# Kernel optimization log

Hardware: AMD Instinct MI355X
Metric: run time of the kernel (lower is better)

Reference implementation:

```python
import jax, jax.numpy as jnp
import numpy as np

WH, WW = 8, 8          # window_size
NUM_HEADS = 16
DIM = 512
NW = 64                # windows per image (mask leading dim)
BATCH = 16             # images
N = WH * WW            # tokens per window


def _relative_position_index():
    coords = np.stack(np.meshgrid(np.arange(WH), np.arange(WW), indexing='ij'))  # (2,Wh,Ww)
    cf = coords.reshape(2, -1)                                                   # (2,N)
    rel = cf[:, :, None] - cf[:, None, :]                                        # (2,N,N)
    rel = rel.transpose(1, 2, 0).astype(np.int64)                                # (N,N,2)
    rel[:, :, 0] += WH - 1
    rel[:, :, 1] += WW - 1
    rel[:, :, 0] *= 2 * WW - 1
    return jnp.asarray(rel.sum(-1), dtype=jnp.int32)                             # (N,N)


def setup_inputs() -> dict:
    key = jax.random.key(0)
    ks = jax.random.split(key, 8)
    B_ = BATCH * NW
    x = jax.random.normal(ks[0], (B_, N, DIM), dtype=jnp.float32)
    # 0 / -100 additive shift-style mask (Swin uses -100.0 for masked pairs)
    mraw = jax.random.uniform(ks[1], (NW, N, N))
    mask = jnp.where(mraw < 0.15, jnp.float32(-100.0), jnp.float32(0.0))
    qkv_w = jax.random.normal(ks[2], (3 * DIM, DIM), dtype=jnp.float32) * (DIM ** -0.5)
    qkv_b = jnp.zeros((3 * DIM,), dtype=jnp.float32)
    proj_w = jax.random.normal(ks[3], (DIM, DIM), dtype=jnp.float32) * (DIM ** -0.5)
    proj_b = jnp.zeros((DIM,), dtype=jnp.float32)
    n_rel = (2 * WH - 1) * (2 * WW - 1)  # 225
    rpb_table = jax.random.normal(ks[4], (n_rel, NUM_HEADS), dtype=jnp.float32) * 0.02
    rel_index = _relative_position_index()
    return {"x": x, "mask": mask, "qkv_w": qkv_w, "qkv_b": qkv_b,
            "proj_w": proj_w, "proj_b": proj_b, "rpb_table": rpb_table,
            "rel_index": rel_index}


def reference(x, mask, qkv_w, qkv_b, proj_w, proj_b, rpb_table, rel_index):
    B_, n, C = x.shape
    H = NUM_HEADS
    hd = C // H
    scale = hd ** -0.5
    qkv = x @ qkv_w.T + qkv_b                       # (B_, N, 3C)
    qkv = qkv.reshape(B_, n, 3, H, hd)
    q = qkv[:, :, 0].transpose(0, 2, 1, 3) * scale  # (B_, H, N, hd)
    k = qkv[:, :, 1].transpose(0, 2, 1, 3)
    v = qkv[:, :, 2].transpose(0, 2, 1, 3)
    attn = jnp.einsum('bhnd,bhmd->bhnm', q, k)      # (B_, H, N, N)
    bias = rpb_table[rel_index.reshape(-1)].reshape(n, n, H).transpose(2, 0, 1)  # (H,N,N)
    attn = attn + bias[None]
    nW = mask.shape[0]
    attn = attn.reshape(B_ // nW, nW, H, n, n) + mask[None, :, None]
    attn = jax.nn.softmax(attn.reshape(B_, H, n, n), axis=-1)
    out = jnp.einsum('bhnm,bhmd->bhnd', attn, v)    # (B_, H, N, hd)
    out = out.transpose(0, 2, 1, 3).reshape(B_, n, C)
    return out @ proj_w.T + proj_b
```

## Files before the change

kernel.cpp:

```cpp
#include <hip/hip_runtime.h>
#include <hip/hip_bf16.h>

typedef unsigned short u16;
typedef __attribute__((ext_vector_type(8))) short bfrag;
typedef __attribute__((ext_vector_type(4))) float ffrag;

#define NWIN_TOT 1024
#define NTOK 64
#define CDIM 512
#define NHEAD 16
#define HDIM 32
#define NW 64

__device__ __forceinline__ u16 f2bf(float f) {
  union { float f; unsigned u; } v; v.f = f;
  unsigned r = v.u + 0x7fffu + ((v.u >> 16) & 1u);
  return (u16)(r >> 16);
}

__device__ __forceinline__ float bfhi2f(unsigned hi_bits) {
  union { unsigned u; float f; } v; v.u = hi_bits; return v.f;
}

__device__ __forceinline__ ffrag mfma16(bfrag a, bfrag b, ffrag c) {
  return __builtin_amdgcn_mfma_f32_16x16x32_bf16(a, b, c, 0, 0, 0);
}

__device__ __forceinline__ void gload16(const u16* src, u16* lds) {
  __builtin_amdgcn_global_load_lds(
      (const __attribute__((address_space(1))) unsigned int*)src,
      (__attribute__((address_space(3))) unsigned int*)lds, 16, 0, 0);
}

#define BAR() __builtin_amdgcn_s_barrier()
#define SCHED0() __builtin_amdgcn_sched_barrier(0)
#define VMW(n) do { asm volatile("s_waitcnt vmcnt(" #n ")" ::: "memory"); \
                    __builtin_amdgcn_sched_barrier(0); } while (0)

__global__ __launch_bounds__(256) void k_prep(const float* __restrict__ x,
                                              const float* __restrict__ qkv_w,
                                              const float* __restrict__ proj_w,
                                              const int*   __restrict__ rel_index,
                                              const float* __restrict__ rpb,
                                              const float* __restrict__ mask,
                                              u16* __restrict__ xb,
                                              u16* __restrict__ wq, u16* __restrict__ wp,
                                              u16* __restrict__ combB) {
  int i = blockIdx.x * 256 + threadIdx.x;
  if (i < 4194304) {
    int e = i * 8;
    const float4* xp = reinterpret_cast<const float4*>(x + e);
    float4 lo = xp[0], hi = xp[1];
    union { u16 u[8]; bfrag v; } pk;
    pk.u[0] = f2bf(lo.x); pk.u[1] = f2bf(lo.y); pk.u[2] = f2bf(lo.z); pk.u[3] = f2bf(lo.w);
    pk.u[4] = f2bf(hi.x); pk.u[5] = f2bf(hi.y); pk.u[6] = f2bf(hi.z); pk.u[7] = f2bf(hi.w);
    *reinterpret_cast<bfrag*>(xb + e) = pk.v;
    return;
  }
  i -= 4194304;
  if (i < 786432) { wq[i] = f2bf(qkv_w[i]); return; }
  i -= 786432;
  if (i < 262144) { wp[i] = f2bf(proj_w[i]); return; }
  i -= 262144;
  {
    int wh = i >> 12, rc = i & 4095;
    int w0 = wh >> 4, h = wh & 15;
    combB[i] = f2bf(rpb[rel_index[rc] * 16 + h] + mask[(w0 << 12) + rc]);
  }
}

#define MFMAQ(mh, nh, BARR) \
  _Pragma("unroll") for (int i_ = 0; i_ < 4; ++i_) \
  _Pragma("unroll") for (int n_ = 0; n_ < 2; ++n_) \
  _Pragma("unroll") for (int ks_ = 0; ks_ < 2; ++ks_) \
    acc[(mh)*4+i_][(nh)*2+n_] = mfma16(a_[i_*2+ks_], BARR[n_*2+ks_], acc[(mh)*4+i_][(nh)*2+n_]);

template<int EPI>
__global__ __launch_bounds__(512, 2) void k_gemm8(const u16* __restrict__ A,
                                                  const u16* __restrict__ W,
                                                  const float* __restrict__ bias,
                                                  u16* __restrict__ qws, u16* __restrict__ kws,
                                                  u16* __restrict__ vws,
                                                  float* __restrict__ out) {
  constexpr int NT = (EPI == 0) ? 6 : 2;
  constexpr int NWG = 256 * NT;
  extern __shared__ __align__(16) u16 smem[];

  const int bid = blockIdx.x;
  const int tile = (bid & 7) * (NWG >> 3) + (bid >> 3);
  const int bn = tile % NT, bm = tile / NT;
  const int brow = bm << 8, bcol = bn << 8;

  const int tid = threadIdx.x;
  const int wv = tid >> 6, lane = tid & 63, c15 = lane & 15, g = lane >> 4;
  const int wr = wv >> 2, wc = wv & 3;
  const int rowA0 = wr * 128 + c15;
  const int rowB0 = wc * 64 + c15;
  const ffrag zf = {0.f, 0.f, 0.f, 0.f};

  ffrag acc[8][4];
#pragma unroll
  for (int i = 0; i < 8; ++i)
#pragma unroll
    for (int n = 0; n < 4; ++n) acc[i][n] = zf;

  auto stage = [&](int t, int mat, int half) {
    u16* db = smem + ((t & 1) * 2 + mat) * 16384 + half * 8192;
    const u16* gsrc = mat ? W : A;
    const int gr0 = (mat ? bcol : brow) + half * 128;
#pragma unroll
    for (int l = 0; l < 2; ++l) {
      int e = l * 4096 + tid * 8;
      int r = e >> 6, cb = (e & 63) << 1;
      int scol = (cb ^ ((r & 7) << 4)) >> 1;
      gload16(gsrc + (size_t)(gr0 + r) * 512 + t * 64 + scol, db + e);
    }
  };

  stage(0, 0, 0); stage(0, 0, 1); stage(0, 1, 0); stage(0, 1, 1);
  stage(1, 0, 0); stage(1, 0, 1); stage(1, 1, 0); stage(1, 1, 1);
  VMW(8);
  BAR();

  bfrag b0_[4];
  {
    const char* B0_ = (const char*)(smem + 1 * 16384);
#pragma unroll
    for (int n = 0; n < 2; ++n) {
      int rb = rowB0 + n * 16;
#pragma unroll
      for (int ks = 0; ks < 2; ++ks)
        b0_[n * 2 + ks] = *(const bfrag*)(B0_ + rb * 128 + ((ks * 64 + g * 16) ^ ((rb & 7) << 4)));
    }
  }

  for (int t = 0; t < 8; ++t) {
    const char* As_ = (const char*)(smem + ((t & 1) * 2 + 0) * 16384);
    const char* Bs_ = (const char*)(smem + ((t & 1) * 2 + 1) * 16384);
    bfrag a_[8], b1_[4];

#pragma unroll
    for (int i = 0; i < 4; ++i) {
      int ra = rowA0 + i * 16;
#pragma unroll
      for (int ks = 0; ks < 2; ++ks)
        a_[i * 2 + ks] = *(const bfrag*)(As_ + ra * 128 + ((ks * 64 + g * 16) ^ ((ra & 7) << 4)));
    }
    BAR();
    __builtin_amdgcn_s_setprio(1);
    MFMAQ(0, 0, b0_);
    __builtin_amdgcn_s_setprio(0);
    BAR();

#pragma unroll
    for (int n = 0; n < 2; ++n) {
      int rb = rowB0 + 32 + n * 16;
#pragma unroll
      for (int ks = 0; ks < 2; ++ks)
        b1_[n * 2 + ks] = *(const bfrag*)(Bs_ + rb * 128 + ((ks * 64 + g * 16) ^ ((rb & 7) << 4)));
    }
    BAR();
    __builtin_amdgcn_s_setprio(1);
    MFMAQ(0, 1, b1_);
    __builtin_amdgcn_s_setprio(0);
    BAR();

#pragma unroll
    for (int i = 0; i < 4; ++i) {
      int ra = rowA0 + 64 + i * 16;
#pragma unroll
      for (int ks = 0; ks < 2; ++ks)
        a_[i * 2 + ks] = *(const bfrag*)(As_ + ra * 128 + ((ks * 64 + g * 16) ^ ((ra & 7) << 4)));
    }
    SCHED0();
    if (t + 2 < 8) { stage(t + 2, 1, 0); stage(t + 2, 1, 1); }
    BAR();
    __builtin_amdgcn_s_setprio(1);
    MFMAQ(1, 1, b1_);
    __builtin_amdgcn_s_setprio(0);
    BAR();

    if (t + 2 < 8) { stage(t + 2, 0, 0); stage(t + 2, 0, 1); }
    if (t < 6) { VMW(8); } else if (t == 6) { VMW(0); }
    BAR();
    __builtin_amdgcn_s_setprio(1);
    MFMAQ(1, 0, b0_);
    __builtin_amdgcn_s_setprio(0);
    if (t < 7) {
      const char* Bn_ = (const char*)(smem + (((t + 1) & 1) * 2 + 1) * 16384);
#pragma unroll
      for (int n = 0; n < 2; ++n) {
        int rb = rowB0 + n * 16;
#pragma unroll
        for (int ks = 0; ks < 2; ++ks)
          b0_[n * 2 + ks] = *(const bfrag*)(Bn_ + rb * 128 + ((ks * 64 + g * 16) ^ ((rb & 7) << 4)));
      }
    }
    BAR();
  }

  if (EPI == 0) {
    const float SCALE = 0.17677669529663687f;
    const int win0 = (brow + wr * 128) >> 6;
#pragma unroll
    for (int n = 0; n < 4; ++n) {
      int c = bcol + wc * 64 + n * 16 + c15;
      float bz = bias[c];
      int which = c >> 9;
      int cq = c & 511, h = cq >> 5, d = cq & 31;
      size_t pb0 = ((size_t)(win0 * NHEAD + h)) << 11;
      size_t pb1 = pb0 + ((size_t)NHEAD << 11);
      if (which == 2) {
        u16* v0 = vws + pb0 + (d << 6);
        u16* v1 = vws + pb1 + (d << 6);
#pragma unroll
        for (int i = 0; i < 8; ++i) {
          u16* vp = (i < 4) ? v0 : v1;
#pragma unroll
          for (int r = 0; r < 4; ++r) {
            int tok = (i & 3) * 16 + g * 4 + r;
            vp[tok] = f2bf(acc[i][n][r] + bz);
          }
        }
      } else {
        const float s = (which == 0) ? SCALE : 1.0f;
        u16* base = (which == 0) ? qws : kws;
        u16* q0 = base + pb0 + d;
        u16* q1 = base + pb1 + d;
#pragma unroll
        for (int i = 0; i < 8; ++i) {
          u16* qp = (i < 4) ? q0 : q1;
#pragma unroll
          for (int r = 0; r < 4; ++r) {
            int tok = (i & 3) * 16 + g * 4 + r;
            qp[tok << 5] = f2bf((acc[i][n][r] + bz) * s);
          }
        }
      }
    }
  } else {
#pragma unroll
    for (int n = 0; n < 4; ++n) {
      int c = bcol + wc * 64 + n * 16 + c15;
      float bz = bias[c];
      float* po = out + (size_t)(brow + wr * 128) * CDIM + c;
#pragma unroll
      for (int i = 0; i < 8; ++i)
#pragma unroll
        for (int r = 0; r < 4; ++r)
          po[(size_t)(i * 16 + g * 4 + r) * CDIM] = acc[i][n][r] + bz;
    }
  }
}

__global__ __launch_bounds__(256) void k_attn(const u16* __restrict__ qws,
                                              const u16* __restrict__ kws,
                                              const u16* __restrict__ vws,
                                              const u16* __restrict__ combB,
                                              u16* __restrict__ yws) {
  __shared__ __align__(16) u16 plds[4][NTOK * NTOK];
  const int tid = threadIdx.x, w = tid >> 6, lane = tid & 63;
  const int c15 = lane & 15, g = lane >> 4, g4 = g * 4;
  const int p = blockIdx.x * 4 + w;
  const int b = p >> 4, h = p & 15;

  const u16* qb_ = qws + (size_t)p * (NTOK * HDIM);
  const u16* kb_ = kws + (size_t)p * (NTOK * HDIM);
  bfrag qa[4], ka[4];
#pragma unroll
  for (int t = 0; t < 4; ++t) {
    qa[t] = *reinterpret_cast<const bfrag*>(qb_ + (t * 16 + c15) * HDIM + g * 8);
    ka[t] = *reinterpret_cast<const bfrag*>(kb_ + (t * 16 + c15) * HDIM + g * 8);
  }

  const u16* cB = combB + ((size_t)(((b & (NW - 1)) << 4) + h) << 12);
  u16* pl = plds[w];
  const ffrag zf = {0.f, 0.f, 0.f, 0.f};

#pragma unroll
  for (int it = 0; it < 4; ++it) {
    int row = it * 16 + c15;
    float l[4][4];
    float mx = -3.0e38f;
#pragma unroll
    for (int jt = 0; jt < 4; ++jt) {
      ffrag s = mfma16(ka[jt], qa[it], zf);
      uint2 cw = *reinterpret_cast<const uint2*>(cB + row * 64 + jt * 16 + g4);
      float c0 = bfhi2f(cw.x << 16);
      float c1 = bfhi2f(cw.x & 0xffff0000u);
      float c2 = bfhi2f(cw.y << 16);
      float c3 = bfhi2f(cw.y & 0xffff0000u);
      l[jt][0] = s[0] + c0;
      l[jt][1] = s[1] + c1;
      l[jt][2] = s[2] + c2;
      l[jt][3] = s[3] + c3;
      mx = fmaxf(mx, fmaxf(fmaxf(l[jt][0], l[jt][1]), fmaxf(l[jt][2], l[jt][3])));
    }
    mx = fmaxf(mx, __shfl_xor(mx, 16));
    mx = fmaxf(mx, __shfl_xor(mx, 32));
    float sum = 0.f;
#pragma unroll
    for (int jt = 0; jt < 4; ++jt)
#pragma unroll
      for (int r = 0; r < 4; ++r) {
        float e = __expf(l[jt][r] - mx);
        l[jt][r] = e;
        sum += e;
      }
    sum += __shfl_xor(sum, 16);
    sum += __shfl_xor(sum, 32);
    float inv = 1.0f / sum;
#pragma unroll
    for (int jt = 0; jt < 4; ++jt) {
      union { u16 u[4]; uint2 v; } pk;
#pragma unroll
      for (int r = 0; r < 4; ++r) pk.u[r] = f2bf(l[jt][r] * inv);
      int off = row * 64 + ((jt * 16 + g4) ^ ((row & 7) << 3));
      *reinterpret_cast<uint2*>(&pl[off]) = pk.v;
    }
  }
  __syncthreads();

  const u16* vb_ = vws + (size_t)p * (HDIM * NTOK);
#pragma unroll
  for (int ct = 0; ct < 2; ++ct) {
    ffrag o[4] = {zf, zf, zf, zf};
#pragma unroll
    for (int ks = 0; ks < 2; ++ks) {
      bfrag vf = *reinterpret_cast<const bfrag*>(vb_ + (ct * 16 + c15) * NTOK + ks * 32 + g * 8);
#pragma unroll
      for (int i = 0; i < 4; ++i) {
        int prow = i * 16 + c15;
        bfrag pa = *reinterpret_cast<const bfrag*>(
            &pl[prow * 64 + ((ks * 32 + g * 8) ^ ((prow & 7) << 3))]);
        o[i] = mfma16(pa, vf, o[i]);
      }
    }
#pragma unroll
    for (int i = 0; i < 4; ++i)
#pragma unroll
      for (int r = 0; r < 4; ++r) {
        int tok = i * 16 + g4 + r;
        yws[((size_t)b * NTOK + tok) * CDIM + h * HDIM + ct * 16 + c15] = f2bf(o[i][r]);
      }
  }
}

extern "C" void kernel_launch(void* const* d_in, const int* in_sizes, int n_in,
                              void* d_out, int out_size, void* d_ws, size_t ws_size,
                              hipStream_t stream) {
  const float* x      = (const float*)d_in[0];
  const float* mask   = (const float*)d_in[1];
  const float* qkv_w  = (const float*)d_in[2];
  const float* qkv_b  = (const float*)d_in[3];
  const float* proj_w = (const float*)d_in[4];
  const float* proj_b = (const float*)d_in[5];
  const float* rpb    = (const float*)d_in[6];
  const int*   rel    = (const int*)d_in[7];
  float* out = (float*)d_out;

  char* ws = (char*)d_ws;
  constexpr size_t SZ_QKV = (size_t)NWIN_TOT * NHEAD * NTOK * HDIM * 2;
  u16* qws = (u16*)(ws);
  u16* kws = (u16*)(ws + SZ_QKV);
  u16* vws = (u16*)(ws + 2 * SZ_QKV);
  u16* xb  = (u16*)(ws + 3 * SZ_QKV);
  u16* yws = xb;
  u16* wq  = (u16*)(ws + 4 * SZ_QKV);
  u16* wp  = (u16*)(ws + 4 * SZ_QKV + 1572864);
  u16* combB = (u16*)(ws + 4 * SZ_QKV + 1572864 + 524288);

  hipFuncSetAttribute((const void*)k_gemm8<0>,
                      hipFuncAttributeMaxDynamicSharedMemorySize, 131072);
  hipFuncSetAttribute((const void*)k_gemm8<1>,
                      hipFuncAttributeMaxDynamicSharedMemorySize, 131072);

  k_prep<<<dim3(36864), dim3(256), 0, stream>>>(x, qkv_w, proj_w, rel, rpb, mask,
                                                xb, wq, wp, combB);
  k_gemm8<0><<<dim3(256 * 6), dim3(512), 131072, stream>>>(xb, wq, qkv_b, qws, kws, vws, nullptr);
  k_attn<<<dim3(NWIN_TOT * NHEAD / 4), dim3(256), 0, stream>>>(qws, kws, vws, combB, yws);
  k_gemm8<1><<<dim3(256 * 2), dim3(512), 131072, stream>>>(yws, wp, proj_b, nullptr, nullptr, nullptr, out);
}
```

Before: 310.3 us.

## Stage QKV and attention outputs through LDS for coalesced vectorized global stores

The QKV GEMM epilogue now writes biased, scaled bf16 results into a swizzled LDS tile, then reads them back so each thread issues 16-byte stores into the Q/K (token-major) and V (transposed) workspaces. The attention kernel also computes both V column tiles in one pass and stages its output through LDS, writing full 128-byte row segments of yws instead of scattered 2-byte stores. This targets the scattered, uncoalesced narrow global writes in both epilogues, at the cost of extra barriers and LDS traffic. It assumes the block-to-column mapping (bn, head0) and the blockIdx-to-(window, head) mapping line up with the tile layouts.

Result: no change. 315.7 us (+1.7%).

```diff
diff --git a/kernel.cpp b/kernel.cpp
--- a/kernel.cpp
+++ b/kernel.cpp
@@ -200,42 +200,59 @@
   }
 
   if (EPI == 0) {
-    const float SCALE = 0.17677669529663687f;
-    const int win0 = (brow + wr * 128) >> 6;
+    const int which = bn >> 1;
+    const int head0 = (bn & 1) * 8;
+    const int win0 = brow >> 6;
+    const float s = (which == 0) ? 0.17677669529663687f : 1.0f;
+    u16* lds16 = smem;
+
 #pragma unroll
     for (int n = 0; n < 4; ++n) {
-      int c = bcol + wc * 64 + n * 16 + c15;
-      float bz = bias[c];
-      int which = c >> 9;
-      int cq = c & 511, h = cq >> 5, d = cq & 31;
-      size_t pb0 = ((size_t)(win0 * NHEAD + h)) << 11;
-      size_t pb1 = pb0 + ((size_t)NHEAD << 11);
-      if (which == 2) {
-        u16* v0 = vws + pb0 + (d << 6);
-        u16* v1 = vws + pb1 + (d << 6);
-#pragma unroll
-        for (int i = 0; i < 8; ++i) {
-          u16* vp = (i < 4) ? v0 : v1;
-#pragma unroll
-          for (int r = 0; r < 4; ++r) {
-            int tok = (i & 3) * 16 + g * 4 + r;
-            vp[tok] = f2bf(acc[i][n][r] + bz);
-          }
+      int colc = wc * 64 + n * 16 + c15;
+      float bz = bias[bcol + colc];
+#pragma unroll
+      for (int i = 0; i < 8; ++i) {
+#pragma unroll
+        for (int r = 0; r < 4; ++r) {
+          int row = wr * 128 + i * 16 + g * 4 + r;
+          int ch = ((colc >> 3) ^ (row & 31)) & 31;
+          lds16[row * 256 + (colc & 7) + (ch << 3)] = f2bf((acc[i][n][r] + bz) * s);
         }
-      } else {
-        const float s = (which == 0) ? SCALE : 1.0f;
-        u16* base = (which == 0) ? qws : kws;
-        u16* q0 = base + pb0 + d;
-        u16* q1 = base + pb1 + d;
-#pragma unroll
-        for (int i = 0; i < 8; ++i) {
-          u16* qp = (i < 4) ? q0 : q1;
-#pragma unroll
-          for (int r = 0; r < 4; ++r) {
-            int tok = (i & 3) * 16 + g * 4 + r;
-            qp[tok << 5] = f2bf((acc[i][n][r] + bz) * s);
-          }
+      }
+    }
+    __syncthreads();
+
+    if (which < 2) {
+      u16* dst = (which == 0) ? qws : kws;
+#pragma unroll
+      for (int it = 0; it < 16; ++it) {
+        int G = it * 512 + tid;
+        int win = G >> 11, rem = G & 2047;
+        int hl = rem >> 8, rem2 = rem & 255;
+        int tok = rem2 >> 2, d0 = (rem2 & 3) << 3;
+        int row = win * 64 + tok, col = hl * 32 + d0;
+        int ch = ((col >> 3) ^ (row & 31)) & 31;
+        bfrag v = *(const bfrag*)(lds16 + row * 256 + (ch << 3));
+        size_t o = ((size_t)((win0 + win) * NHEAD + head0 + hl) * NTOK + tok) * HDIM + d0;
+        *(bfrag*)(dst + o) = v;
+      }
+    } else {
+#pragma unroll
+      for (int it = 0; it < 16; ++it) {
+        int G = it * 512 + tid;
+        int win = G >> 11, rem = G & 2047;
+        int hl = rem >> 8, rem2 = rem & 255;
+        int d = rem2 >> 3, tok0 = (rem2 & 7) << 3;
+        int col = hl * 32 + d;
+        union { u16 u[8]; bfrag v; } pk;
+#pragma unroll
+        for (int j = 0; j < 8; ++j) {
+          int row = win * 64 + tok0 + j;
+          int ch = ((col >> 3) ^ (row & 31)) & 31;
+          pk.u[j] = lds16[row * 256 + (col & 7) + (ch << 3)];
         }
+        size_t o = ((size_t)((win0 + win) * NHEAD + head0 + hl) * HDIM + d) * NTOK + tok0;
+        *(bfrag*)(vws + o) = pk.v;
       }
     }
   } else {
@@ -286,14 +303,10 @@
     for (int jt = 0; jt < 4; ++jt) {
       ffrag s = mfma16(ka[jt], qa[it], zf);
       uint2 cw = *reinterpret_cast<const uint2*>(cB + row * 64 + jt * 16 + g4);
-      float c0 = bfhi2f(cw.x << 16);
-      float c1 = bfhi2f(cw.x & 0xffff0000u);
-      float c2 = bfhi2f(cw.y << 16);
-      float c3 = bfhi2f(cw.y & 0xffff0000u);
-      l[jt][0] = s[0] + c0;
-      l[jt][1] = s[1] + c1;
-      l[jt][2] = s[2] + c2;
-      l[jt][3] = s[3] + c3;
+      l[jt][0] = s[0] + bfhi2f(cw.x << 16);
+      l[jt][1] = s[1] + bfhi2f(cw.x & 0xffff0000u);
+      l[jt][2] = s[2] + bfhi2f(cw.y << 16);
+      l[jt][3] = s[3] + bfhi2f(cw.y & 0xffff0000u);
       mx = fmaxf(mx, fmaxf(fmaxf(l[jt][0], l[jt][1]), fmaxf(l[jt][2], l[jt][3])));
     }
     mx = fmaxf(mx, __shfl_xor(mx, 16));
@@ -322,27 +335,46 @@
   __syncthreads();
 
   const u16* vb_ = vws + (size_t)p * (HDIM * NTOK);
-#pragma unroll
-  for (int ct = 0; ct < 2; ++ct) {
-    ffrag o[4] = {zf, zf, zf, zf};
-#pragma unroll
-    for (int ks = 0; ks < 2; ++ks) {
-      bfrag vf = *reinterpret_cast<const bfrag*>(vb_ + (ct * 16 + c15) * NTOK + ks * 32 + g * 8);
-#pragma unroll
-      for (int i = 0; i < 4; ++i) {
-        int prow = i * 16 + c15;
-        bfrag pa = *reinterpret_cast<const bfrag*>(
-            &pl[prow * 64 + ((ks * 32 + g * 8) ^ ((prow & 7) << 3))]);
-        o[i] = mfma16(pa, vf, o[i]);
-      }
-    }
-#pragma unroll
-    for (int i = 0; i < 4; ++i)
-#pragma unroll
-      for (int r = 0; r < 4; ++r) {
-        int tok = i * 16 + g4 + r;
-        yws[((size_t)b * NTOK + tok) * CDIM + h * HDIM + ct * 16 + c15] = f2bf(o[i][r]);
-      }
+  ffrag o0[4] = {zf, zf, zf, zf}, o1[4] = {zf, zf, zf, zf};
+#pragma unroll
+  for (int ks = 0; ks < 2; ++ks) {
+    bfrag vf0 = *reinterpret_cast<const bfrag*>(vb_ + c15 * NTOK + ks * 32 + g * 8);
+    bfrag vf1 = *reinterpret_cast<const bfrag*>(vb_ + (16 + c15) * NTOK + ks * 32 + g * 8);
+#pragma unroll
+    for (int i = 0; i < 4; ++i) {
+      int prow = i * 16 + c15;
+      bfrag pa = *reinterpret_cast<const bfrag*>(
+          &pl[prow * 64 + ((ks * 32 + g * 8) ^ ((prow & 7) << 3))]);
+      o0[i] = mfma16(pa, vf0, o0[i]);
+      o1[i] = mfma16(pa, vf1, o1[i]);
+    }
+  }
+  __syncthreads();
+
+  u16* yl = &plds[0][0];
+#pragma unroll
+  for (int i = 0; i < 4; ++i)
+#pragma unroll
+    for (int r = 0; r < 4; ++r) {
+      int tok = i * 16 + g4 + r;
+      yl[tok * 136 + w * 32 + c15] = f2bf(o0[i][r]);
+      yl[tok * 136 + w * 32 + 16 + c15] = f2bf(o1[i][r]);
+    }
+  __syncthreads();
+  {
+    const int b2 = blockIdx.x >> 2;
+    const int h0 = (blockIdx.x * 4) & 15;
+    int row = tid >> 2, seg = tid & 3;
+    const u16* src = yl + row * 136 + seg * 32;
+    u16* dst = yws + ((size_t)b2 * NTOK + row) * CDIM + h0 * HDIM + seg * 32;
+    bfrag v0 = *(const bfrag*)(src);
+    bfrag v1 = *(const bfrag*)(src + 8);
+    bfrag v2 = *(const bfrag*)(src + 16);
+    bfrag v3 = *(const bfrag*)(src + 24);
+    *(bfrag*)(dst) = v0;
+    *(bfrag*)(dst + 8) = v1;
+    *(bfrag*)(dst + 16) = v2;
+    *(bfrag*)(dst + 24) = v3;
   }
 }
 
```

## Fuse window attention with output projection GEMM in one kernel

Applied to the files above, without the earlier changes.

Merges the attention kernel and the projection GEMM into a single kernel where each 512-thread block handles one window: eight waves each compute two heads of attention, write the bf16 output into LDS, then all waves run the 64x512x512 projection reading proj weights straight from global memory. This removes the global round-trip of the attention output and one kernel launch. In exchange, occupancy falls to one block per CU because of the roughly 130KB LDS footprint. The projection weights are re-read from global/L2 per window with no LDS staging, and the tuned pipelined GEMM is replaced by a simple unpipelined loop.

Result: slower. 330.9 us (+6.6%).

```diff
diff --git a/kernel.cpp b/kernel.cpp
--- a/kernel.cpp
+++ b/kernel.cpp
@@ -75,14 +75,12 @@
   _Pragma("unroll") for (int ks_ = 0; ks_ < 2; ++ks_) \
     acc[(mh)*4+i_][(nh)*2+n_] = mfma16(a_[i_*2+ks_], BARR[n_*2+ks_], acc[(mh)*4+i_][(nh)*2+n_]);
 
-template<int EPI>
 __global__ __launch_bounds__(512, 2) void k_gemm8(const u16* __restrict__ A,
                                                   const u16* __restrict__ W,
                                                   const float* __restrict__ bias,
                                                   u16* __restrict__ qws, u16* __restrict__ kws,
-                                                  u16* __restrict__ vws,
-                                                  float* __restrict__ out) {
-  constexpr int NT = (EPI == 0) ? 6 : 2;
+                                                  u16* __restrict__ vws) {
+  constexpr int NT = 6;
   constexpr int NWG = 256 * NT;
   extern __shared__ __align__(16) u16 smem[];
 
@@ -199,7 +197,7 @@
     BAR();
   }
 
-  if (EPI == 0) {
+  {
     const float SCALE = 0.17677669529663687f;
     const int win0 = (brow + wr * 128) >> 6;
 #pragma unroll
@@ -238,102 +236,90 @@
         }
       }
     }
-  } else {
-#pragma unroll
-    for (int n = 0; n < 4; ++n) {
-      int c = bcol + wc * 64 + n * 16 + c15;
-      float bz = bias[c];
-      float* po = out + (size_t)(brow + wr * 128) * CDIM + c;
-#pragma unroll
-      for (int i = 0; i < 8; ++i)
-#pragma unroll
-        for (int r = 0; r < 4; ++r)
-          po[(size_t)(i * 16 + g * 4 + r) * CDIM] = acc[i][n][r] + bz;
-    }
-  }
-}
-
-__global__ __launch_bounds__(256) void k_attn(const u16* __restrict__ qws,
-                                              const u16* __restrict__ kws,
-                                              const u16* __restrict__ vws,
-                                              const u16* __restrict__ combB,
-                                              u16* __restrict__ yws) {
-  __shared__ __align__(16) u16 plds[4][NTOK * NTOK];
+  }
+}
+
+__global__ __launch_bounds__(512, 1) void k_attn_proj(const u16* __restrict__ qws,
+                                                      const u16* __restrict__ kws,
+                                                      const u16* __restrict__ vws,
+                                                      const u16* __restrict__ combB,
+                                                      const u16* __restrict__ wp,
+                                                      const float* __restrict__ proj_b,
+                                                      float* __restrict__ out) {
+  extern __shared__ __align__(16) u16 sm2[];
+  u16* yl = sm2;
   const int tid = threadIdx.x, w = tid >> 6, lane = tid & 63;
   const int c15 = lane & 15, g = lane >> 4, g4 = g * 4;
-  const int p = blockIdx.x * 4 + w;
-  const int b = p >> 4, h = p & 15;
-
-  const u16* qb_ = qws + (size_t)p * (NTOK * HDIM);
-  const u16* kb_ = kws + (size_t)p * (NTOK * HDIM);
-  bfrag qa[4], ka[4];
-#pragma unroll
-  for (int t = 0; t < 4; ++t) {
-    qa[t] = *reinterpret_cast<const bfrag*>(qb_ + (t * 16 + c15) * HDIM + g * 8);
-    ka[t] = *reinterpret_cast<const bfrag*>(kb_ + (t * 16 + c15) * HDIM + g * 8);
-  }
-
-  const u16* cB = combB + ((size_t)(((b & (NW - 1)) << 4) + h) << 12);
-  u16* pl = plds[w];
+  u16* pl = sm2 + 33280 + w * 4096;
+  const int b = blockIdx.x;
   const ffrag zf = {0.f, 0.f, 0.f, 0.f};
 
-#pragma unroll
-  for (int it = 0; it < 4; ++it) {
-    int row = it * 16 + c15;
-    float l[4][4];
-    float mx = -3.0e38f;
-#pragma unroll
-    for (int jt = 0; jt < 4; ++jt) {
-      ffrag s = mfma16(ka[jt], qa[it], zf);
-      uint2 cw = *reinterpret_cast<const uint2*>(cB + row * 64 + jt * 16 + g4);
-      float c0 = bfhi2f(cw.x << 16);
-      float c1 = bfhi2f(cw.x & 0xffff0000u);
-      float c2 = bfhi2f(cw.y << 16);
-      float c3 = bfhi2f(cw.y & 0xffff0000u);
-      l[jt][0] = s[0] + c0;
-      l[jt][1] = s[1] + c1;
-      l[jt][2] = s[2] + c2;
-      l[jt][3] = s[3] + c3;
-      mx = fmaxf(mx, fmaxf(fmaxf(l[jt][0], l[jt][1]), fmaxf(l[jt][2], l[jt][3])));
-    }
-    mx = fmaxf(mx, __shfl_xor(mx, 16));
-    mx = fmaxf(mx, __shfl_xor(mx, 32));
-    float sum = 0.f;
-#pragma unroll
-    for (int jt = 0; jt < 4; ++jt)
-#pragma unroll
-      for (int r = 0; r < 4; ++r) {
-        float e = __expf(l[jt][r] - mx);
-        l[jt][r] = e;
-        sum += e;
-      }
-    sum += __shfl_xor(sum, 16);
-    sum += __shfl_xor(sum, 32);
-    float inv = 1.0f / sum;
-#pragma unroll
-    for (int jt = 0; jt < 4; ++jt) {
-      union { u16 u[4]; uint2 v; } pk;
-#pragma unroll
-      for (int r = 0; r < 4; ++r) pk.u[r] = f2bf(l[jt][r] * inv);
-      int off = row * 64 + ((jt * 16 + g4) ^ ((row & 7) << 3));
-      *reinterpret_cast<uint2*>(&pl[off]) = pk.v;
-    }
-  }
-  __syncthreads();
-
-  const u16* vb_ = vws + (size_t)p * (HDIM * NTOK);
-#pragma unroll
-  for (int ct = 0; ct < 2; ++ct) {
-    ffrag o[4] = {zf, zf, zf, zf};
+  for (int hh = 0; hh < 2; ++hh) {
+    const int h = w * 2 + hh;
+    const int p = b * NHEAD + h;
+
+    const u16* qb_ = qws + (size_t)p * (NTOK * HDIM);
+    const u16* kb_ = kws + (size_t)p * (NTOK * HDIM);
+    bfrag qa[4], ka[4];
+#pragma unroll
+    for (int t = 0; t < 4; ++t) {
+      qa[t] = *reinterpret_cast<const bfrag*>(qb_ + (t * 16 + c15) * HDIM + g * 8);
+      ka[t] = *reinterpret_cast<const bfrag*>(kb_ + (t * 16 + c15) * HDIM + g * 8);
+    }
+    const u16* cB = combB + ((size_t)(((b & (NW - 1)) << 4) + h) << 12);
+
+#pragma unroll
+    for (int it = 0; it < 4; ++it) {
+      int row = it * 16 + c15;
+      float l[4][4];
+      float mx = -3.0e38f;
+#pragma unroll
+      for (int jt = 0; jt < 4; ++jt) {
+        ffrag s = mfma16(ka[jt], qa[it], zf);
+        uint2 cw = *reinterpret_cast<const uint2*>(cB + row * 64 + jt * 16 + g4);
+        l[jt][0] = s[0] + bfhi2f(cw.x << 16);
+        l[jt][1] = s[1] + bfhi2f(cw.x & 0xffff0000u);
+        l[jt][2] = s[2] + bfhi2f(cw.y << 16);
+        l[jt][3] = s[3] + bfhi2f(cw.y & 0xffff0000u);
+        mx = fmaxf(mx, fmaxf(fmaxf(l[jt][0], l[jt][1]), fmaxf(l[jt][2], l[jt][3])));
+      }
+      mx = fmaxf(mx, __shfl_xor(mx, 16));
+      mx = fmaxf(mx, __shfl_xor(mx, 32));
+      float sum = 0.f;
+#pragma unroll
+      for (int jt = 0; jt < 4; ++jt)
+#pragma unroll
+        for (int r = 0; r < 4; ++r) {
+          float e = __expf(l[jt][r] - mx);
+          l[jt][r] = e;
+          sum += e;
+        }
+      sum += __shfl_xor(sum, 16);
+      sum += __shfl_xor(sum, 32);
+      float inv = 1.0f / sum;
+#pragma unroll
+      for (int jt = 0; jt < 4; ++jt) {
+        union { u16 u[4]; uint2 v; } pk;
+#pragma unroll
+        for (int r = 0; r < 4; ++r) pk.u[r] = f2bf(l[jt][r] * inv);
+        int off = row * 64 + ((jt * 16 + g4) ^ ((row & 7) << 3));
+        *reinterpret_cast<uint2*>(&pl[off]) = pk.v;
+      }
+    }
+
+    const u16* vb_ = vws + (size_t)p * (HDIM * NTOK);
+    ffrag o0[4] = {zf, zf, zf, zf}, o1[4] = {zf, zf, zf, zf};
 #pragma unroll
     for (int ks = 0; ks < 2; ++ks) {
-      bfrag vf = *reinterpret_cast<const bfrag*>(vb_ + (ct * 16 + c15) * NTOK + ks * 32 + g * 8);
+      bfrag vf0 = *reinterpret_cast<const bfrag*>(vb_ + c15 * NTOK + ks * 32 + g * 8);
+      bfrag vf1 = *reinterpret_cast<const bfrag*>(vb_ + (16 + c15) * NTOK + ks * 32 + g * 8);
 #pragma unroll
       for (int i = 0; i < 4; ++i) {
         int prow = i * 16 + c15;
         bfrag pa = *reinterpret_cast<const bfrag*>(
             &pl[prow * 64 + ((ks * 32 + g * 8) ^ ((prow & 7) << 3))]);
-        o[i] = mfma16(pa, vf, o[i]);
+        o0[i] = mfma16(pa, vf0, o0[i]);
+        o1[i] = mfma16(pa, vf1, o1[i]);
       }
     }
 #pragma unroll
@@ -341,8 +327,43 @@
 #pragma unroll
       for (int r = 0; r < 4; ++r) {
         int tok = i * 16 + g4 + r;
-        yws[((size_t)b * NTOK + tok) * CDIM + h * HDIM + ct * 16 + c15] = f2bf(o[i][r]);
-      }
+        yl[tok * 520 + h * 32 + c15] = f2bf(o0[i][r]);
+        yl[tok * 520 + h * 32 + 16 + c15] = f2bf(o1[i][r]);
+      }
+  }
+  __syncthreads();
+
+  ffrag acc[4][4];
+#pragma unroll
+  for (int i = 0; i < 4; ++i)
+#pragma unroll
+    for (int n = 0; n < 4; ++n) acc[i][n] = zf;
+
+  for (int ks = 0; ks < 16; ++ks) {
+    bfrag a_[4], b_[4];
+#pragma unroll
+    for (int i = 0; i < 4; ++i)
+      a_[i] = *reinterpret_cast<const bfrag*>(yl + (i * 16 + c15) * 520 + ks * 32 + g * 8);
+#pragma unroll
+    for (int n = 0; n < 4; ++n)
+      b_[n] = *reinterpret_cast<const bfrag*>(wp + (size_t)(w * 64 + n * 16 + c15) * 512 + ks * 32 + g * 8);
+#pragma unroll
+    for (int i = 0; i < 4; ++i)
+#pragma unroll
+      for (int n = 0; n < 4; ++n)
+        acc[i][n] = mfma16(a_[i], b_[n], acc[i][n]);
+  }
+
+#pragma unroll
+  for (int n = 0; n < 4; ++n) {
+    int c = w * 64 + n * 16 + c15;
+    float bz = proj_b[c];
+    float* po = out + (size_t)b * NTOK * CDIM + c;
+#pragma unroll
+    for (int i = 0; i < 4; ++i)
+#pragma unroll
+      for (int r = 0; r < 4; ++r)
+        po[(size_t)(i * 16 + g4 + r) * CDIM] = acc[i][n][r] + bz;
   }
 }
 
@@ -365,19 +386,18 @@
   u16* kws = (u16*)(ws + SZ_QKV);
   u16* vws = (u16*)(ws + 2 * SZ_QKV);
   u16* xb  = (u16*)(ws + 3 * SZ_QKV);
-  u16* yws = xb;
   u16* wq  = (u16*)(ws + 4 * SZ_QKV);
   u16* wp  = (u16*)(ws + 4 * SZ_QKV + 1572864);
   u16* combB = (u16*)(ws + 4 * SZ_QKV + 1572864 + 524288);
 
-  hipFuncSetAttribute((const void*)k_gemm8<0>,
+  hipFuncSetAttribute((const void*)k_gemm8,
                       hipFuncAttributeMaxDynamicSharedMemorySize, 131072);
-  hipFuncSetAttribute((const void*)k_gemm8<1>,
-                      hipFuncAttributeMaxDynamicSharedMemorySize, 131072);
+  hipFuncSetAttribute((const void*)k_attn_proj,
+                      hipFuncAttributeMaxDynamicSharedMemorySize, 132096);
 
   k_prep<<<dim3(36864), dim3(256), 0, stream>>>(x, qkv_w, proj_w, rel, rpb, mask,
                                                 xb, wq, wp, combB);
-  k_gemm8<0><<<dim3(256 * 6), dim3(512), 131072, stream>>>(xb, wq, qkv_b, qws, kws, vws, nullptr);
-  k_attn<<<dim3(NWIN_TOT * NHEAD / 4), dim3(256), 0, stream>>>(qws, kws, vws, combB, yws);
-  k_gemm8<1><<<dim3(256 * 2), dim3(512), 131072, stream>>>(yws, wp, proj_b, nullptr, nullptr, nullptr, out);
-}
+  k_gemm8<<<dim3(256 * 6), dim3(512), 131072, stream>>>(xb, wq, qkv_b, qws, kws, vws);
+  k_attn_proj<<<dim3(NWIN_TOT), dim3(512), 132096, stream>>>(qws, kws, vws, combB,
+                                                             wp, proj_b, out);
+}
```

## Make GEMM workgroups loop over all column tiles; stage attention output in LDS

Applied to the files above, without the earlier changes.

Both GEMM kernels now launch one workgroup per 256-row block (256 workgroups). Each workgroup loops over every 256-column tile, keeping the double-buffered load pipeline running across tiles and writing each tile's epilogue as it finishes. The goal is to save per-workgroup launch and prologue cost and keep A-rows resident in L2, at the price of a single wave of 256 workgroups with launch_bounds occupancy 1, so parallelism and latency hiding may drop. The attention kernel also computes both V column tiles together and stages the output in LDS, so it can write yws with coalesced 16-byte stores instead of scattered 2-byte stores.

Result: slower. 416.1 us (+34.1%).

```diff
diff --git a/kernel.cpp b/kernel.cpp
--- a/kernel.cpp
+++ b/kernel.cpp
@@ -76,20 +76,19 @@
     acc[(mh)*4+i_][(nh)*2+n_] = mfma16(a_[i_*2+ks_], BARR[n_*2+ks_], acc[(mh)*4+i_][(nh)*2+n_]);
 
 template<int EPI>
-__global__ __launch_bounds__(512, 2) void k_gemm8(const u16* __restrict__ A,
+__global__ __launch_bounds__(512, 1) void k_gemmp(const u16* __restrict__ A,
                                                   const u16* __restrict__ W,
                                                   const float* __restrict__ bias,
                                                   u16* __restrict__ qws, u16* __restrict__ kws,
                                                   u16* __restrict__ vws,
                                                   float* __restrict__ out) {
   constexpr int NT = (EPI == 0) ? 6 : 2;
-  constexpr int NWG = 256 * NT;
+  constexpr int NS = NT * 8;
   extern __shared__ __align__(16) u16 smem[];
 
   const int bid = blockIdx.x;
-  const int tile = (bid & 7) * (NWG >> 3) + (bid >> 3);
-  const int bn = tile % NT, bm = tile / NT;
-  const int brow = bm << 8, bcol = bn << 8;
+  const int bm = (bid & 7) * 32 + (bid >> 3);
+  const int brow = bm << 8;
 
   const int tid = threadIdx.x;
   const int wv = tid >> 6, lane = tid & 63, c15 = lane & 15, g = lane >> 4;
@@ -104,16 +103,17 @@
 #pragma unroll
     for (int n = 0; n < 4; ++n) acc[i][n] = zf;
 
-  auto stage = [&](int t, int mat, int half) {
-    u16* db = smem + ((t & 1) * 2 + mat) * 16384 + half * 8192;
+  auto stage = [&](int sg, int mat, int half) {
+    u16* db = smem + ((sg & 1) * 2 + mat) * 16384 + half * 8192;
     const u16* gsrc = mat ? W : A;
-    const int gr0 = (mat ? bcol : brow) + half * 128;
+    const int gr0 = (mat ? ((sg >> 3) << 8) : brow) + half * 128;
+    const int kc = (sg & 7) * 64;
 #pragma unroll
     for (int l = 0; l < 2; ++l) {
       int e = l * 4096 + tid * 8;
       int r = e >> 6, cb = (e & 63) << 1;
       int scol = (cb ^ ((r & 7) << 4)) >> 1;
-      gload16(gsrc + (size_t)(gr0 + r) * 512 + t * 64 + scol, db + e);
+      gload16(gsrc + (size_t)(gr0 + r) * 512 + kc + scol, db + e);
     }
   };
 
@@ -134,121 +134,132 @@
     }
   }
 
-  for (int t = 0; t < 8; ++t) {
-    const char* As_ = (const char*)(smem + ((t & 1) * 2 + 0) * 16384);
-    const char* Bs_ = (const char*)(smem + ((t & 1) * 2 + 1) * 16384);
-    bfrag a_[8], b1_[4];
-
-#pragma unroll
-    for (int i = 0; i < 4; ++i) {
-      int ra = rowA0 + i * 16;
-#pragma unroll
-      for (int ks = 0; ks < 2; ++ks)
-        a_[i * 2 + ks] = *(const bfrag*)(As_ + ra * 128 + ((ks * 64 + g * 16) ^ ((ra & 7) << 4)));
-    }
-    BAR();
-    __builtin_amdgcn_s_setprio(1);
-    MFMAQ(0, 0, b0_);
-    __builtin_amdgcn_s_setprio(0);
-    BAR();
-
-#pragma unroll
-    for (int n = 0; n < 2; ++n) {
-      int rb = rowB0 + 32 + n * 16;
-#pragma unroll
-      for (int ks = 0; ks < 2; ++ks)
-        b1_[n * 2 + ks] = *(const bfrag*)(Bs_ + rb * 128 + ((ks * 64 + g * 16) ^ ((rb & 7) << 4)));
-    }
-    BAR();
-    __builtin_amdgcn_s_setprio(1);
-    MFMAQ(0, 1, b1_);
-    __builtin_amdgcn_s_setprio(0);
-    BAR();
-
-#pragma unroll
-    for (int i = 0; i < 4; ++i) {
-      int ra = rowA0 + 64 + i * 16;
-#pragma unroll
-      for (int ks = 0; ks < 2; ++ks)
-        a_[i * 2 + ks] = *(const bfrag*)(As_ + ra * 128 + ((ks * 64 + g * 16) ^ ((ra & 7) << 4)));
-    }
-    SCHED0();
-    if (t + 2 < 8) { stage(t + 2, 1, 0); stage(t + 2, 1, 1); }
-    BAR();
-    __builtin_amdgcn_s_setprio(1);
-    MFMAQ(1, 1, b1_);
-    __builtin_amdgcn_s_setprio(0);
-    BAR();
-
-    if (t + 2 < 8) { stage(t + 2, 0, 0); stage(t + 2, 0, 1); }
-    if (t < 6) { VMW(8); } else if (t == 6) { VMW(0); }
-    BAR();
-    __builtin_amdgcn_s_setprio(1);
-    MFMAQ(1, 0, b0_);
-    __builtin_amdgcn_s_setprio(0);
-    if (t < 7) {
-      const char* Bn_ = (const char*)(smem + (((t + 1) & 1) * 2 + 1) * 16384);
+  for (int j = 0; j < NT; ++j) {
+    for (int t = 0; t < 8; ++t) {
+      const int s = j * 8 + t;
+      const char* As_ = (const char*)(smem + ((s & 1) * 2 + 0) * 16384);
+      const char* Bs_ = (const char*)(smem + ((s & 1) * 2 + 1) * 16384);
+      bfrag a_[8], b1_[4];
+
+#pragma unroll
+      for (int i = 0; i < 4; ++i) {
+        int ra = rowA0 + i * 16;
+#pragma unroll
+        for (int ks = 0; ks < 2; ++ks)
+          a_[i * 2 + ks] = *(const bfrag*)(As_ + ra * 128 + ((ks * 64 + g * 16) ^ ((ra & 7) << 4)));
+      }
+      BAR();
+      __builtin_amdgcn_s_setprio(1);
+      MFMAQ(0, 0, b0_);
+      __builtin_amdgcn_s_setprio(0);
+      BAR();
+
 #pragma unroll
       for (int n = 0; n < 2; ++n) {
-        int rb = rowB0 + n * 16;
+        int rb = rowB0 + 32 + n * 16;
 #pragma unroll
         for (int ks = 0; ks < 2; ++ks)
-          b0_[n * 2 + ks] = *(const bfrag*)(Bn_ + rb * 128 + ((ks * 64 + g * 16) ^ ((rb & 7) << 4)));
-      }
-    }
-    BAR();
-  }
-
-  if (EPI == 0) {
-    const float SCALE = 0.17677669529663687f;
-    const int win0 = (brow + wr * 128) >> 6;
-#pragma unroll
-    for (int n = 0; n < 4; ++n) {
-      int c = bcol + wc * 64 + n * 16 + c15;
-      float bz = bias[c];
-      int which = c >> 9;
-      int cq = c & 511, h = cq >> 5, d = cq & 31;
-      size_t pb0 = ((size_t)(win0 * NHEAD + h)) << 11;
-      size_t pb1 = pb0 + ((size_t)NHEAD << 11);
-      if (which == 2) {
-        u16* v0 = vws + pb0 + (d << 6);
-        u16* v1 = vws + pb1 + (d << 6);
-#pragma unroll
-        for (int i = 0; i < 8; ++i) {
-          u16* vp = (i < 4) ? v0 : v1;
-#pragma unroll
-          for (int r = 0; r < 4; ++r) {
-            int tok = (i & 3) * 16 + g * 4 + r;
-            vp[tok] = f2bf(acc[i][n][r] + bz);
+          b1_[n * 2 + ks] = *(const bfrag*)(Bs_ + rb * 128 + ((ks * 64 + g * 16) ^ ((rb & 7) << 4)));
+      }
+      BAR();
+      __builtin_amdgcn_s_setprio(1);
+      MFMAQ(0, 1, b1_);
+      __builtin_amdgcn_s_setprio(0);
+      BAR();
+
+#pragma unroll
+      for (int i = 0; i < 4; ++i) {
+        int ra = rowA0 + 64 + i * 16;
+#pragma unroll
+        for (int ks = 0; ks < 2; ++ks)
+          a_[i * 2 + ks] = *(const bfrag*)(As_ + ra * 128 + ((ks * 64 + g * 16) ^ ((ra & 7) << 4)));
+      }
+      SCHED0();
+      if (s + 2 < NS) { stage(s + 2, 1, 0); stage(s + 2, 1, 1); }
+      BAR();
+      __builtin_amdgcn_s_setprio(1);
+      MFMAQ(1, 1, b1_);
+      __builtin_amdgcn_s_setprio(0);
+      BAR();
+
+      if (s + 2 < NS) { stage(s + 2, 0, 0); stage(s + 2, 0, 1); }
+      if (s < NS - 2) { VMW(8); } else if (s == NS - 2) { VMW(0); }
+      BAR();
+      __builtin_amdgcn_s_setprio(1);
+      MFMAQ(1, 0, b0_);
+      __builtin_amdgcn_s_setprio(0);
+      if (s + 1 < NS) {
+        const char* Bn_ = (const char*)(smem + (((s + 1) & 1) * 2 + 1) * 16384);
+#pragma unroll
+        for (int n = 0; n < 2; ++n) {
+          int rb = rowB0 + n * 16;
+#pragma unroll
+          for (int ks = 0; ks < 2; ++ks)
+            b0_[n * 2 + ks] = *(const bfrag*)(Bn_ + rb * 128 + ((ks * 64 + g * 16) ^ ((rb & 7) << 4)));
+        }
+      }
+      BAR();
+    }
+
+    const int bcol = j << 8;
+    if (EPI == 0) {
+      const float SCALE = 0.17677669529663687f;
+      const int win0 = (brow + wr * 128) >> 6;
+#pragma unroll
+      for (int n = 0; n < 4; ++n) {
+        int c = bcol + wc * 64 + n * 16 + c15;
+        float bz = bias[c];
+        int which = c >> 9;
+        int cq = c & 511, h = cq >> 5, d = cq & 31;
+        size_t pb0 = ((size_t)(win0 * NHEAD + h)) << 11;
+        size_t pb1 = pb0 + ((size_t)NHEAD << 11);
+        if (which == 2) {
+          u16* v0 = vws + pb0 + (d << 6);
+          u16* v1 = vws + pb1 + (d << 6);
+#pragma unroll
+          for (int i = 0; i < 8; ++i) {
+            u16* vp = (i < 4) ? v0 : v1;
+#pragma unroll
+            for (int r = 0; r < 4; ++r) {
+              int tok = (i & 3) * 16 + g * 4 + r;
+              vp[tok] = f2bf(acc[i][n][r] + bz);
+            }
+          }
+        } else {
+          const float s2 = (which == 0) ? SCALE : 1.0f;
+          u16* base = (which == 0) ? qws : kws;
+          u16* q0 = base + pb0 + d;
+          u16* q1 = base + pb1 + d;
+#pragma unroll
+          for (int i = 0; i < 8; ++i) {
+            u16* qp = (i < 4) ? q0 : q1;
+#pragma unroll
+            for (int r = 0; r < 4; ++r) {
+              int tok = (i & 3) * 16 + g * 4 + r;
+              qp[tok << 5] = f2bf((acc[i][n][r] + bz) * s2);
+            }
           }
         }
-      } else {
-        const float s = (which == 0) ? SCALE : 1.0f;
-        u16* base = (which == 0) ? qws : kws;
-        u16* q0 = base + pb0 + d;
-        u16* q1 = base + pb1 + d;
-#pragma unroll
-        for (int i = 0; i < 8; ++i) {
-          u16* qp = (i < 4) ? q0 : q1;
-#pragma unroll
-          for (int r = 0; r < 4; ++r) {
-            int tok = (i & 3) * 16 + g * 4 + r;
-            qp[tok << 5] = f2bf((acc[i][n][r] + bz) * s);
-          }
-        }
-      }
-    }
-  } else {
-#pragma unroll
-    for (int n = 0; n < 4; ++n) {
-      int c = bcol + wc * 64 + n * 16 + c15;
-      float bz = bias[c];
-      float* po = out + (size_t)(brow + wr * 128) * CDIM + c;
+      }
+    } else {
+#pragma unroll
+      for (int n = 0; n < 4; ++n) {
+        int c = bcol + wc * 64 + n * 16 + c15;
+        float bz = bias[c];
+        float* po = out + (size_t)(brow + wr * 128) * CDIM + c;
+#pragma unroll
+        for (int i = 0; i < 8; ++i)
+#pragma unroll
+          for (int r = 0; r < 4; ++r)
+            po[(size_t)(i * 16 + g * 4 + r) * CDIM] = acc[i][n][r] + bz;
+      }
+    }
+
+    if (j + 1 < NT) {
 #pragma unroll
       for (int i = 0; i < 8; ++i)
 #pragma unroll
-        for (int r = 0; r < 4; ++r)
-          po[(size_t)(i * 16 + g * 4 + r) * CDIM] = acc[i][n][r] + bz;
+        for (int n = 0; n < 4; ++n) acc[i][n] = zf;
     }
   }
 }
@@ -286,14 +297,10 @@
     for (int jt = 0; jt < 4; ++jt) {
       ffrag s = mfma16(ka[jt], qa[it], zf);
       uint2 cw = *reinterpret_cast<const uint2*>(cB + row * 64 + jt * 16 + g4);
-      float c0 = bfhi2f(cw.x << 16);
-      float c1 = bfhi2f(cw.x & 0xffff0000u);
-      float c2 = bfhi2f(cw.y << 16);
-      float c3 = bfhi2f(cw.y & 0xffff0000u);
-      l[jt][0] = s[0] + c0;
-      l[jt][1] = s[1] + c1;
-      l[jt][2] = s[2] + c2;
-      l[jt][3] = s[3] + c3;
+      l[jt][0] = s[0] + bfhi2f(cw.x << 16);
+      l[jt][1] = s[1] + bfhi2f(cw.x & 0xffff0000u);
+      l[jt][2] = s[2] + bfhi2f(cw.y << 16);
+      l[jt][3] = s[3] + bfhi2f(cw.y & 0xffff0000u);
       mx = fmaxf(mx, fmaxf(fmaxf(l[jt][0], l[jt][1]), fmaxf(l[jt][2], l[jt][3])));
     }
     mx = fmaxf(mx, __shfl_xor(mx, 16));
@@ -322,27 +329,46 @@
   __syncthreads();
 
   const u16* vb_ = vws + (size_t)p * (HDIM * NTOK);
-#pragma unroll
-  for (int ct = 0; ct < 2; ++ct) {
-    ffrag o[4] = {zf, zf, zf, zf};
-#pragma unroll
-    for (int ks = 0; ks < 2; ++ks) {
-      bfrag vf = *reinterpret_cast<const bfrag*>(vb_ + (ct * 16 + c15) * NTOK + ks * 32 + g * 8);
-#pragma unroll
-      for (int i = 0; i < 4; ++i) {
-        int prow = i * 16 + c15;
-        bfrag pa = *reinterpret_cast<const bfrag*>(
-            &pl[prow * 64 + ((ks * 32 + g * 8) ^ ((prow & 7) << 3))]);
-        o[i] = mfma16(pa, vf, o[i]);
-      }
-    }
-#pragma unroll
-    for (int i = 0; i < 4; ++i)
-#pragma unroll
-      for (int r = 0; r < 4; ++r) {
-        int tok = i * 16 + g4 + r;
-        yws[((size_t)b * NTOK + tok) * CDIM + h * HDIM + ct * 16 + c15] = f2bf(o[i][r]);
-      }
+  ffrag o0[4] = {zf, zf, zf, zf}, o1[4] = {zf, zf, zf, zf};
+#pragma unroll
+  for (int ks = 0; ks < 2; ++ks) {
+    bfrag vf0 = *reinterpret_cast<const bfrag*>(vb_ + c15 * NTOK + ks * 32 + g * 8);
+    bfrag vf1 = *reinterpret_cast<const bfrag*>(vb_ + (16 + c15) * NTOK + ks * 32 + g * 8);
+#pragma unroll
+    for (int i = 0; i < 4; ++i) {
+      int prow = i * 16 + c15;
+      bfrag pa = *reinterpret_cast<const bfrag*>(
+          &pl[prow * 64 + ((ks * 32 + g * 8) ^ ((prow & 7) << 3))]);
+      o0[i] = mfma16(pa, vf0, o0[i]);
+      o1[i] = mfma16(pa, vf1, o1[i]);
+    }
+  }
+  __syncthreads();
+
+  u16* yl = &plds[0][0];
+#pragma unroll
+  for (int i = 0; i < 4; ++i)
+#pragma unroll
+    for (int r = 0; r < 4; ++r) {
+      int tok = i * 16 + g4 + r;
+      yl[tok * 136 + w * 32 + c15] = f2bf(o0[i][r]);
+      yl[tok * 136 + w * 32 + 16 + c15] = f2bf(o1[i][r]);
+    }
+  __syncthreads();
+  {
+    const int b2 = blockIdx.x >> 2;
+    const int h0 = (blockIdx.x * 4) & 15;
+    int row = tid >> 2, seg = tid & 3;
+    const u16* src = yl + row * 136 + seg * 32;
+    u16* dst = yws + ((size_t)b2 * NTOK + row) * CDIM + h0 * HDIM + seg * 32;
+    bfrag v0 = *(const bfrag*)(src);
+    bfrag v1 = *(const bfrag*)(src + 8);
+    bfrag v2 = *(const bfrag*)(src + 16);
+    bfrag v3 = *(const bfrag*)(src + 24);
+    *(bfrag*)(dst) = v0;
+    *(bfrag*)(dst + 8) = v1;
+    *(bfrag*)(dst + 16) = v2;
+    *(bfrag*)(dst + 24) = v3;
   }
 }
 
@@ -370,14 +396,14 @@
   u16* wp  = (u16*)(ws + 4 * SZ_QKV + 1572864);
   u16* combB = (u16*)(ws + 4 * SZ_QKV + 1572864 + 524288);
 
-  hipFuncSetAttribute((const void*)k_gemm8<0>,
+  hipFuncSetAttribute((const void*)k_gemmp<0>,
                       hipFuncAttributeMaxDynamicSharedMemorySize, 131072);
-  hipFuncSetAttribute((const void*)k_gemm8<1>,
+  hipFuncSetAttribute((const void*)k_gemmp<1>,
                       hipFuncAttributeMaxDynamicSharedMemorySize, 131072);
 
   k_prep<<<dim3(36864), dim3(256), 0, stream>>>(x, qkv_w, proj_w, rel, rpb, mask,
                                                 xb, wq, wp, combB);
-  k_gemm8<0><<<dim3(256 * 6), dim3(512), 131072, stream>>>(xb, wq, qkv_b, qws, kws, vws, nullptr);
+  k_gemmp<0><<<dim3(256), dim3(512), 131072, stream>>>(xb, wq, qkv_b, qws, kws, vws, nullptr);
   k_attn<<<dim3(NWIN_TOT * NHEAD / 4), dim3(256), 0, stream>>>(qws, kws, vws, combB, yws);
-  k_gemm8<1><<<dim3(256 * 2), dim3(512), 131072, stream>>>(yws, wp, proj_b, nullptr, nullptr, nullptr, out);
-}
+  k_gemmp<1><<<dim3(256), dim3(512), 131072, stream>>>(yws, wp, proj_b, nullptr, nullptr, nullptr, out);
+}
```
